# Kernel tuning notes

Hardware: AMD Instinct MI355X
Metric: run time of the kernel (lower is better)

Reference implementation:

```python
import jax, jax.numpy as jnp
import numpy as np

N_VAR, N_CON, N_SOC = 100_000, 100_000, 20_000
E_VC, E_SC = 2_000_000, 300_000
H = 64


def setup_inputs() -> dict:
    key = jax.random.key(0)
    ks = iter(jax.random.split(key, 64))

    def rn(shape, s=0.05):
        return jax.random.normal(next(ks), shape, jnp.float32) * s

    inp = {
        "var_x": rn((N_VAR, 7), 1.0),
        "con_x": rn((N_CON, 4), 1.0),
        "soc_x": rn((N_SOC, 6), 1.0),
        "W_var": rn((7, H)), "b_var": jnp.zeros((H,), jnp.float32),
        "W_con": rn((4, H)), "b_con": jnp.zeros((H,), jnp.float32),
        "W_soc": rn((6, H)), "b_soc": jnp.zeros((H,), jnp.float32),
    }
    for l in ("l1", "l2"):
        for d in ("f", "b"):
            inp[f"{l}{d}_Wp"] = rn((H, H))
            inp[f"{l}{d}_bp"] = jnp.zeros((H,), jnp.float32)
            inp[f"{l}{d}_Ws"] = rn((H, H))
            inp[f"{l}{d}_Wn"] = rn((H, H))
            inp[f"{l}{d}_b"] = jnp.zeros((H,), jnp.float32)
    inp["W_hid"] = rn((H, H)); inp["b_hid"] = jnp.zeros((H,), jnp.float32)
    inp["W_out"] = rn((H, 1)); inp["b_out"] = jnp.zeros((1,), jnp.float32)
    inp["vc_src"] = jax.random.randint(next(ks), (E_VC,), 0, N_VAR)
    inp["vc_dst"] = jax.random.randint(next(ks), (E_VC,), 0, N_CON)
    inp["sc_src"] = jax.random.randint(next(ks), (E_SC,), 0, N_SOC)
    inp["sc_dst"] = jax.random.randint(next(ks), (E_SC,), 0, N_CON)
    return inp


def _sage_pool(x_src, x_dst, src, dst, n_dst, Wp, bp, Ws, Wn, b):
    """DGL SAGEConv(aggregator_type='pool') on one bipartite relation.

    max-pool of relu(fc_pool(src feats)) over in-edges, then fc_self + fc_neigh + bias.
    """
    pooled = jax.nn.relu(x_src @ Wp + bp)                       # [N_src, H]
    agg = jax.ops.segment_max(pooled[src], dst, num_segments=n_dst)  # [N_dst, H]
    agg = jnp.where(jnp.isfinite(agg), agg, 0.0)                # zero in-degree -> 0 (DGL semantics)
    return x_dst @ Ws + agg @ Wn + b


def reference(var_x, con_x, soc_x,
              W_var, b_var, W_con, b_con, W_soc, b_soc,
              l1f_Wp, l1f_bp, l1f_Ws, l1f_Wn, l1f_b,
              l1b_Wp, l1b_bp, l1b_Ws, l1b_Wn, l1b_b,
              l2f_Wp, l2f_bp, l2f_Ws, l2f_Wn, l2f_b,
              l2b_Wp, l2b_bp, l2b_Ws, l2b_Wn, l2b_b,
              W_hid, b_hid, W_out, b_out,
              vc_src, vc_dst, sc_src, sc_dst):
    n_var, n_con, n_soc = var_x.shape[0], con_x.shape[0], soc_x.shape[0]

    # PreNormLayer with beta=0, sigma=1 (non-trainable, no pretrain update) is identity.
    h_var = jax.nn.relu(var_x @ W_var + b_var)
    h_con = jax.nn.relu(con_x @ W_con + b_con)
    h_soc = jax.nn.relu(soc_x @ W_soc + b_soc)

    # Each conv layer shares one SAGEConv for {v2c, s2c} and one for {c2v, c2s}.
    layers = [
        ((l1f_Wp, l1f_bp, l1f_Ws, l1f_Wn, l1f_b), (l1b_Wp, l1b_bp, l1b_Ws, l1b_Wn, l1b_b)),
        ((l2f_Wp, l2f_bp, l2f_Ws, l2f_Wn, l2f_b), (l2b_Wp, l2b_bp, l2b_Ws, l2b_Wn, l2b_b)),
    ]

    # n_passes = 1
    # forward half-pass: update constraint nodes; HeteroGraphConv sums v2c and s2c outputs.
    for fwd, _ in layers:
        c = (_sage_pool(h_var, h_con, vc_src, vc_dst, n_con, *fwd)
             + _sage_pool(h_soc, h_con, sc_src, sc_dst, n_con, *fwd))
        h_con = jax.nn.relu(c)
    # backward half-pass: update var and soc nodes from constraints (c2v, c2s = reversed edges).
    for _, bwd in layers:
        v = _sage_pool(h_con, h_var, vc_dst, vc_src, n_var, *bwd)
        s = _sage_pool(h_con, h_soc, sc_dst, sc_src, n_soc, *bwd)
        h_var = jax.nn.relu(v)
        h_soc = jax.nn.relu(s)

    # Output MLP: [Linear, ReLU]*2 in the source duplicates ONE shared Linear module.
    z = h_var
    for _ in range(2):
        z = jax.nn.relu(z @ W_hid + b_hid)
    return z @ W_out + b_out  # [n_var, 1] per-variable logits (readout_op=None)
```

## Files before the change

kernel.cpp:

```cpp
#include <hip/hip_runtime.h>

#define NV 100000
#define NC 100000
#define NSOC 20000
#define NVS (NV + NSOC)
#define EVC 2000000
#define ESC 300000
#define H 64

constexpr int BSH = 7;
constexpr int NBMAX = 1024;
constexpr int EPB = 8192;

template<int K1, int NSEC, bool RELU, int TR>
__global__ __launch_bounds__(256) void gemm_lds(
    const float* X1, const float* __restrict__ W1,
    const float* __restrict__ X2, const float* __restrict__ W2,
    const float* __restrict__ bias, float* out,
    int N, float s1)
{
  __shared__ __align__(16) float sx1[TR * K1];
  __shared__ __align__(16) float sx2[NSEC ? TR * H : 4];

  const int n0 = blockIdx.x * TR;

  if constexpr ((K1 & 3) == 0) {
    const float4* X4 = reinterpret_cast<const float4*>(X1);
    float4* S4 = reinterpret_cast<float4*>(sx1);
    const long base4 = (long)n0 * K1 / 4;
    const long lim4 = (long)N * K1 / 4;
    for (int i = threadIdx.x; i < TR * K1 / 4; i += 256)
      S4[i] = (base4 + i < lim4) ? X4[base4 + i] : make_float4(0.f, 0.f, 0.f, 0.f);
  } else {
    const long base = (long)n0 * K1;
    const long lim = (long)N * K1;
    for (int i = threadIdx.x; i < TR * K1; i += 256)
      sx1[i] = (base + i < lim) ? X1[base + i] : 0.f;
  }
  if constexpr (NSEC) {
    const float4* X4 = reinterpret_cast<const float4*>(X2);
    float4* S4 = reinterpret_cast<float4*>(sx2);
    const long base4 = (long)n0 * H / 4;
    const long lim4 = (long)N * H / 4;
    for (int i = threadIdx.x; i < TR * H / 4; i += 256)
      S4[i] = (base4 + i < lim4) ? X4[base4 + i] : make_float4(0.f, 0.f, 0.f, 0.f);
  }
  __syncthreads();

  const int lane = threadIdx.x & 63;
  const int wv = threadIdx.x >> 6;

  float w1[K1];
#pragma unroll
  for (int k = 0; k < K1; ++k) w1[k] = W1[k * H + lane];
  float w2[NSEC ? H : 1];
  if constexpr (NSEC) {
#pragma unroll
    for (int k = 0; k < H; ++k) w2[k] = W2[k * H + lane];
  }
  const float bj = bias[lane];

  constexpr int RPW = TR / 4;
  const int r0 = wv * RPW;

  if constexpr (K1 == H) {
    for (int i = 0; i < RPW; i += 2) {
      const int na = n0 + r0 + i;
      if (na >= N) break;
      const bool wb = (na + 1) < N;

      const float4* xa = reinterpret_cast<const float4*>(sx1 + (r0 + i) * H);
      const float4* xb = reinterpret_cast<const float4*>(sx1 + (r0 + i + 1) * H);
      float a0 = 0.f, a1 = 0.f, a2 = 0.f, a3 = 0.f;
      float b0 = 0.f, b1 = 0.f, b2 = 0.f, b3 = 0.f;
#pragma unroll
      for (int k4 = 0; k4 < H / 4; ++k4) {
        const float4 va = xa[k4];
        const float4 vb = xb[k4];
        a0 = fmaf(va.x, w1[4 * k4 + 0], a0);
        b0 = fmaf(vb.x, w1[4 * k4 + 0], b0);
        a1 = fmaf(va.y, w1[4 * k4 + 1], a1);
        b1 = fmaf(vb.y, w1[4 * k4 + 1], b1);
        a2 = fmaf(va.z, w1[4 * k4 + 2], a2);
        b2 = fmaf(vb.z, w1[4 * k4 + 2], b2);
        a3 = fmaf(va.w, w1[4 * k4 + 3], a3);
        b3 = fmaf(vb.w, w1[4 * k4 + 3], b3);
      }
      float accA = s1 * (((a0 + a1) + (a2 + a3)) + bj);
      float accB = s1 * (((b0 + b1) + (b2 + b3)) + bj);

      if constexpr (NSEC) {
        const float4* ya = reinterpret_cast<const float4*>(sx2 + (r0 + i) * H);
        const float4* yb = reinterpret_cast<const float4*>(sx2 + (r0 + i + 1) * H);
        a0 = 0.f; a1 = 0.f; a2 = 0.f; a3 = 0.f;
        b0 = 0.f; b1 = 0.f; b2 = 0.f; b3 = 0.f;
#pragma unroll
        for (int k4 = 0; k4 < H / 4; ++k4) {
          const float4 va = ya[k4];
          const float4 vb = yb[k4];
          a0 = fmaf(va.x, w2[4 * k4 + 0], a0);
          b0 = fmaf(vb.x, w2[4 * k4 + 0], b0);
          a1 = fmaf(va.y, w2[4 * k4 + 1], a1);
          b1 = fmaf(vb.y, w2[4 * k4 + 1], b1);
          a2 = fmaf(va.z, w2[4 * k4 + 2], a2);
          b2 = fmaf(vb.z, w2[4 * k4 + 2], b2);
          a3 = fmaf(va.w, w2[4 * k4 + 3], a3);
          b3 = fmaf(vb.w, w2[4 * k4 + 3], b3);
        }
        accA += (a0 + a1) + (a2 + a3);
        accB += (b0 + b1) + (b2 + b3);
      }

      if constexpr (RELU) { accA = fmaxf(accA, 0.f); accB = fmaxf(accB, 0.f); }
      out[(size_t)na * H + lane] = accA;
      if (wb) out[(size_t)(na + 1) * H + lane] = accB;
    }
  } else {
    for (int i = 0; i < RPW; i += 2) {
      const int na = n0 + r0 + i;
      if (na >= N) break;
      const bool wb = (na + 1) < N;
      const float* xa = sx1 + (r0 + i) * K1;
      const float* xb = sx1 + (r0 + i + 1) * K1;
      float accA = 0.f, accB = 0.f;
#pragma unroll
      for (int k = 0; k < K1; ++k) {
        accA = fmaf(xa[k], w1[k], accA);
        accB = fmaf(xb[k], w1[k], accB);
      }
      accA = s1 * (accA + bj);
      accB = s1 * (accB + bj);
      if constexpr (RELU) { accA = fmaxf(accA, 0.f); accB = fmaxf(accB, 0.f); }
      out[(size_t)na * H + lane] = accA;
      if (wb) out[(size_t)(na + 1) * H + lane] = accB;
    }
  }
}

template<int TR>
__global__ __launch_bounds__(256) void dualgemm_k(
    const float* __restrict__ X, const float* __restrict__ Wa,
    const float* __restrict__ ba, const float* __restrict__ Wb,
    const float* __restrict__ bb, float* __restrict__ out, int N)
{
  __shared__ __align__(16) float sx[TR * H];
  const int n0 = blockIdx.x * TR;
  {
    const float4* X4 = reinterpret_cast<const float4*>(X);
    float4* S4 = reinterpret_cast<float4*>(sx);
    const long base4 = (long)n0 * (H / 4);
    const long lim4 = (long)N * (H / 4);
    for (int i = threadIdx.x; i < TR * H / 4; i += 256)
      S4[i] = (base4 + i < lim4) ? X4[base4 + i] : make_float4(0.f, 0.f, 0.f, 0.f);
  }
  __syncthreads();

  const int lane = threadIdx.x & 63;
  const int wv = threadIdx.x >> 6;
  float wA[H], wB[H];
#pragma unroll
  for (int k = 0; k < H; ++k) { wA[k] = Wa[k * H + lane]; wB[k] = Wb[k * H + lane]; }
  const float bja = ba[lane];
  const float bjb = bb[lane];

  constexpr int RPW = TR / 4;
  const int r0 = wv * RPW;
  for (int i = 0; i < RPW; i += 2) {
    const int na = n0 + r0 + i;
    if (na >= N) break;
    const bool hasB = (na + 1) < N;

    const float4* xa = reinterpret_cast<const float4*>(sx + (r0 + i) * H);
    const float4* xb = reinterpret_cast<const float4*>(sx + (r0 + i + 1) * H);
    float pa0 = 0.f, pa1 = 0.f, pa2 = 0.f, pa3 = 0.f;
    float pb0 = 0.f, pb1 = 0.f, pb2 = 0.f, pb3 = 0.f;
    float qa0 = 0.f, qa1 = 0.f, qa2 = 0.f, qa3 = 0.f;
    float qb0 = 0.f, qb1 = 0.f, qb2 = 0.f, qb3 = 0.f;
#pragma unroll
    for (int k4 = 0; k4 < H / 4; ++k4) {
      const float4 va = xa[k4];
      const float4 vb = xb[k4];
      pa0 = fmaf(va.x, wA[4 * k4 + 0], pa0);
      pb0 = fmaf(vb.x, wA[4 * k4 + 0], pb0);
      qa0 = fmaf(va.x, wB[4 * k4 + 0], qa0);
      qb0 = fmaf(vb.x, wB[4 * k4 + 0], qb0);
      pa1 = fmaf(va.y, wA[4 * k4 + 1], pa1);
      pb1 = fmaf(vb.y, wA[4 * k4 + 1], pb1);
      qa1 = fmaf(va.y, wB[4 * k4 + 1], qa1);
      qb1 = fmaf(vb.y, wB[4 * k4 + 1], qb1);
      pa2 = fmaf(va.z, wA[4 * k4 + 2], pa2);
      pb2 = fmaf(vb.z, wA[4 * k4 + 2], pb2);
      qa2 = fmaf(va.z, wB[4 * k4 + 2], qa2);
      qb2 = fmaf(vb.z, wB[4 * k4 + 2], qb2);
      pa3 = fmaf(va.w, wA[4 * k4 + 3], pa3);
      pb3 = fmaf(vb.w, wA[4 * k4 + 3], pb3);
      qa3 = fmaf(va.w, wB[4 * k4 + 3], qa3);
      qb3 = fmaf(vb.w, wB[4 * k4 + 3], qb3);
    }
    const float accAa = fmaxf((pa0 + pa1) + (pa2 + pa3) + bja, 0.f);
    const float accAb = fmaxf((qa0 + qa1) + (qa2 + qa3) + bjb, 0.f);
    out[(size_t)na * 128 + lane] = accAa;
    out[(size_t)na * 128 + 64 + lane] = accAb;
    if (hasB) {
      const float accBa = fmaxf((pb0 + pb1) + (pb2 + pb3) + bja, 0.f);
      const float accBb = fmaxf((qb0 + qb1) + (qb2 + qb3) + bjb, 0.f);
      out[(size_t)(na + 1) * 128 + lane] = accBa;
      out[(size_t)(na + 1) * 128 + 64 + lane] = accBb;
    }
  }
}

template<int TR>
__global__ __launch_bounds__(256) void mlp_k(
    const float* __restrict__ X, const float* __restrict__ W,
    const float* __restrict__ bh, const float* __restrict__ Wout,
    const float* __restrict__ bo, float* __restrict__ out, int N)
{
  __shared__ __align__(16) float sx[TR * H];
  __shared__ __align__(16) float sz[4][H];

  const int n0 = blockIdx.x * TR;
  {
    const float4* X4 = reinterpret_cast<const float4*>(X);
    float4* S4 = reinterpret_cast<float4*>(sx);
    const long base4 = (long)n0 * H / 4;
    const long lim4 = (long)N * H / 4;
    for (int i = threadIdx.x; i < TR * H / 4; i += 256)
      S4[i] = (base4 + i < lim4) ? X4[base4 + i] : make_float4(0.f, 0.f, 0.f, 0.f);
  }
  __syncthreads();

  const int lane = threadIdx.x & 63;
  const int wv = threadIdx.x >> 6;
  float w[H];
#pragma unroll
  for (int k = 0; k < H; ++k) w[k] = W[k * H + lane];
  const float bhl = bh[lane];
  const float wo = Wout[lane];
  const float bol = bo[0];

  constexpr int RPW = TR / 4;
  const int r0 = wv * RPW;
  for (int i = 0; i < RPW; ++i) {
    const int n = n0 + r0 + i;
    if (n >= N) break;
    const float4* x4 = reinterpret_cast<const float4*>(sx + (r0 + i) * H);
    float a0 = 0.f, a1 = 0.f, a2 = 0.f, a3 = 0.f;
#pragma unroll
    for (int k4 = 0; k4 < H / 4; ++k4) {
      const float4 v = x4[k4];
      a0 = fmaf(v.x, w[4 * k4 + 0], a0);
      a1 = fmaf(v.y, w[4 * k4 + 1], a1);
      a2 = fmaf(v.z, w[4 * k4 + 2], a2);
      a3 = fmaf(v.w, w[4 * k4 + 3], a3);
    }
    const float z1 = fmaxf((a0 + a1) + (a2 + a3) + bhl, 0.f);
    sz[wv][lane] = z1;
    const float4* z4 = reinterpret_cast<const float4*>(sz[wv]);
    a0 = 0.f; a1 = 0.f; a2 = 0.f; a3 = 0.f;
#pragma unroll
    for (int k4 = 0; k4 < H / 4; ++k4) {
      const float4 v = z4[k4];
      a0 = fmaf(v.x, w[4 * k4 + 0], a0);
      a1 = fmaf(v.y, w[4 * k4 + 1], a1);
      a2 = fmaf(v.z, w[4 * k4 + 2], a2);
      a3 = fmaf(v.w, w[4 * k4 + 3], a3);
    }
    const float z2 = fmaxf((a0 + a1) + (a2 + a3) + bhl, 0.f);
    float v = z2 * wo;
#pragma unroll
    for (int off = 32; off; off >>= 1) v += __shfl_down(v, off);
    if (lane == 0) out[n] = v + bol;
  }
}

__global__ __launch_bounds__(256) void bhist_k(const int* __restrict__ key,
                                               int* __restrict__ bcnt, int E, int nb) {
  __shared__ int h[NBMAX];
  for (int i = threadIdx.x; i < nb; i += 256) h[i] = 0;
  __syncthreads();
  const int base = blockIdx.x * EPB;
  for (int i = threadIdx.x; i < EPB; i += 256) {
    const int e = base + i;
    if (e < E) atomicAdd(&h[key[e] >> BSH], 1);
  }
  __syncthreads();
  for (int i = threadIdx.x; i < nb; i += 256)
    if (h[i]) atomicAdd(&bcnt[i], h[i]);
}

__global__ __launch_bounds__(1024) void bscan_k(const int* __restrict__ bcnt,
                                                int* __restrict__ bcur,
                                                int* __restrict__ sbase, int nb) {
  __shared__ int s[1024];
  const int t = threadIdx.x;
  const int v = (t < nb) ? bcnt[t] : 0;
  s[t] = v;
  __syncthreads();
  for (int off = 1; off < 1024; off <<= 1) {
    int x = (t >= off) ? s[t - off] : 0;
    __syncthreads();
    s[t] += x;
    __syncthreads();
  }
  if (t < nb) {
    const int ex = s[t] - v;
    bcur[t] = ex;
    sbase[t] = ex;
    if (t == nb - 1) sbase[nb] = s[t];
  }
}

__global__ __launch_bounds__(256) void bscatter_k(
    const int* __restrict__ key, const int* __restrict__ payload,
    int* __restrict__ bcur, int2* __restrict__ sorted, int E, int nb) {
  __shared__ int h[NBMAX];
  __shared__ int gb[NBMAX];
  __shared__ unsigned short lr[EPB];
  for (int i = threadIdx.x; i < nb; i += 256) h[i] = 0;
  __syncthreads();
  const int base = blockIdx.x * EPB;
  for (int i = threadIdx.x; i < EPB; i += 256) {
    const int e = base + i;
    if (e < E) lr[i] = (unsigned short)atomicAdd(&h[key[e] >> BSH], 1);
  }
  __syncthreads();
  for (int i = threadIdx.x; i < nb; i += 256)
    if (h[i]) gb[i] = atomicAdd(&bcur[i], h[i]);
  __syncthreads();
  for (int i = threadIdx.x; i < EPB; i += 256) {
    const int e = base + i;
    if (e < E) {
      const int k = key[e];
      sorted[gb[k >> BSH] + lr[i]] = make_int2(k, payload[e]);
    }
  }
}

__global__ __launch_bounds__(256) void bfinish_k(
    const int2* __restrict__ sorted, const int* __restrict__ sbase,
    int* __restrict__ rp, int* __restrict__ ei, int Nn) {
  __shared__ int cnt[128];
  __shared__ int scn[128];
  const int b = blockIdx.x;
  const int node0 = b << BSH;
  const int e0 = sbase[b], e1 = sbase[b + 1];
  const int t = threadIdx.x;
  if (t < 128) cnt[t] = 0;
  __syncthreads();
  for (int e = e0 + t; e < e1; e += 256)
    atomicAdd(&cnt[sorted[e].x - node0], 1);
  __syncthreads();
  if (t < 128) scn[t] = cnt[t];
  __syncthreads();
#pragma unroll
  for (int off = 1; off < 128; off <<= 1) {
    int v = (t < 128 && t >= off) ? scn[t - off] : 0;
    __syncthreads();
    if (t < 128) scn[t] += v;
    __syncthreads();
  }
  const int nInB = (Nn - node0 < 128) ? (Nn - node0) : 128;
  int myexcl = 0;
  if (t < 128) myexcl = scn[t] - cnt[t];
  if (t < nInB) rp[node0 + t] = e0 + myexcl;
  if (b == (int)gridDim.x - 1 && t == 0) rp[Nn] = e1;
  __syncthreads();
  if (t < 128) cnt[t] = myexcl;
  __syncthreads();
  for (int e = e0 + t; e < e1; e += 256) {
    const int2 kp = sorted[e];
    const int p = atomicAdd(&cnt[kp.x - node0], 1);
    ei[e0 + p] = kp.y;
  }
}

__device__ __forceinline__ float4 fmax4(float4 a, float4 b) {
  return make_float4(fmaxf(a.x, b.x), fmaxf(a.y, b.y),
                     fmaxf(a.z, b.z), fmaxf(a.w, b.w));
}

__device__ __forceinline__ float4 gmax2_csr(const float4* __restrict__ t4,
                                            const int* __restrict__ rp,
                                            const int* __restrict__ ei,
                                            int n, int g, int sub) {
  const int p0 = rp[n], p1 = rp[n + 1];
  const float4 z = make_float4(0.f, 0.f, 0.f, 0.f);
  float4 m0 = z, m1 = z, m2 = z, m3 = z, m4 = z, m5 = z, m6 = z, m7 = z;
  if (p1 > p0) {
    const int last = p1 - 1;
    for (int p = p0; p < p1; p += 16) {
      int e0 = p + 0 + g;  e0 = e0 <= last ? e0 : last;
      int e1 = p + 2 + g;  e1 = e1 <= last ? e1 : last;
      int e2 = p + 4 + g;  e2 = e2 <= last ? e2 : last;
      int e3 = p + 6 + g;  e3 = e3 <= last ? e3 : last;
      int e4 = p + 8 + g;  e4 = e4 <= last ? e4 : last;
      int e5 = p + 10 + g; e5 = e5 <= last ? e5 : last;
      int e6 = p + 12 + g; e6 = e6 <= last ? e6 : last;
      int e7 = p + 14 + g; e7 = e7 <= last ? e7 : last;
      const int s0 = ei[e0], s1 = ei[e1], s2 = ei[e2], s3 = ei[e3];
      const int s4 = ei[e4], s5 = ei[e5], s6 = ei[e6], s7 = ei[e7];
      m0 = fmax4(m0, t4[(size_t)s0 * 32 + sub]);
      m1 = fmax4(m1, t4[(size_t)s1 * 32 + sub]);
      m2 = fmax4(m2, t4[(size_t)s2 * 32 + sub]);
      m3 = fmax4(m3, t4[(size_t)s3 * 32 + sub]);
      m4 = fmax4(m4, t4[(size_t)s4 * 32 + sub]);
      m5 = fmax4(m5, t4[(size_t)s5 * 32 + sub]);
      m6 = fmax4(m6, t4[(size_t)s6 * 32 + sub]);
      m7 = fmax4(m7, t4[(size_t)s7 * 32 + sub]);
    }
  }
  float4 m = fmax4(fmax4(fmax4(m0, m1), fmax4(m2, m3)),
                   fmax4(fmax4(m4, m5), fmax4(m6, m7)));
  m.x = fmaxf(m.x, __shfl_xor(m.x, 32));
  m.y = fmaxf(m.y, __shfl_xor(m.y, 32));
  m.z = fmaxf(m.z, __shfl_xor(m.z, 32));
  m.w = fmaxf(m.w, __shfl_xor(m.w, 32));
  return m;
}

__global__ __launch_bounds__(256) void gather2f_k(
    const float4* __restrict__ t4,
    const int* __restrict__ rpCv, const int* __restrict__ eiCv,
    const int* __restrict__ rpCs, const int* __restrict__ eiCs,
    float4* __restrict__ agg1, float4* __restrict__ agg2, int N)
{
  const int lane = threadIdx.x & 63;
  const int g = lane >> 5, sub = lane & 31;
  const int n = __builtin_amdgcn_readfirstlane(blockIdx.x * 4 + (threadIdx.x >> 6));
  if (n >= N) return;
  const float4 a = gmax2_csr(t4, rpCv, eiCv, n, g, sub);
  const float4 b = gmax2_csr(t4 + (size_t)NV * 32, rpCs, eiCs, n, g, sub);
  const float4 r = make_float4(a.x + b.x, a.y + b.y, a.z + b.z, a.w + b.w);
  if (g == 0) {
    if (sub < 16) agg1[(size_t)n * 16 + sub] = r;
    else          agg2[(size_t)n * 16 + (sub - 16)] = r;
  }
}

__global__ __launch_bounds__(256) void gathervs2_k(
    const float4* __restrict__ t4,
    const int* __restrict__ rpV, const int* __restrict__ eiV,
    const int* __restrict__ rpS, const int* __restrict__ eiS,
    float4* __restrict__ agg1, float4* __restrict__ agg2)
{
  const int lane = threadIdx.x & 63;
  const int g = lane >> 5, sub = lane & 31;
  const int n = __builtin_amdgcn_readfirstlane(blockIdx.x * 4 + (threadIdx.x >> 6));
  if (n >= NVS) return;
  float4 m;
  if (n < NV) m = gmax2_csr(t4, rpV, eiV, n, g, sub);
  else        m = gmax2_csr(t4, rpS, eiS, n - NV, g, sub);
  if (g == 0) {
    if (sub < 16) agg1[(size_t)n * 16 + sub] = m;
    else          agg2[(size_t)n * 16 + (sub - 16)] = m;
  }
}

extern "C" void kernel_launch(void* const* d_in, const int* in_sizes, int n_in,
                              void* d_out, int out_size, void* d_ws, size_t ws_size,
                              hipStream_t stream) {
  const float* var_x = (const float*)d_in[0];
  const float* con_x = (const float*)d_in[1];
  const float* soc_x = (const float*)d_in[2];
  const float* W_var = (const float*)d_in[3];
  const float* b_var = (const float*)d_in[4];
  const float* W_con = (const float*)d_in[5];
  const float* b_con = (const float*)d_in[6];
  const float* W_soc = (const float*)d_in[7];
  const float* b_soc = (const float*)d_in[8];
  const float* L[4][5];
  for (int l = 0; l < 4; ++l)
    for (int p = 0; p < 5; ++p)
      L[l][p] = (const float*)d_in[9 + l * 5 + p];
  const float* W_hid = (const float*)d_in[29];
  const float* b_hid = (const float*)d_in[30];
  const float* W_out = (const float*)d_in[31];
  const float* b_out = (const float*)d_in[32];
  const int* vc_src = (const int*)d_in[33];
  const int* vc_dst = (const int*)d_in[34];
  const int* sc_src = (const int*)d_in[35];
  const int* sc_dst = (const int*)d_in[36];

  char* ws = (char*)d_ws;
  const size_t F_VS = (size_t)NVS * H * 4;
  const size_t F_C  = (size_t)NC * H * 4;
  float* hvs   = (float*)(ws);
  float* h_con = (float*)(ws + F_VS);
  float* bufA  = (float*)(ws + F_VS + F_C);
  float* bufB  = (float*)(ws + 3 * F_VS + F_C);
  int2*  sorted = (int2*)bufB;
  char* csr = ws + 3 * F_VS + 3 * F_C;
  int* rpCv = (int*)(csr);
  int* eiCv = rpCv + (NC + 1);
  int* rpCs = eiCv + EVC;
  int* eiCs = rpCs + (NC + 1);
  int* rpV  = eiCs + ESC;
  int* eiV  = rpV + (NV + 1);
  int* rpS  = eiV + EVC;
  int* eiS  = rpS + (NSOC + 1);
  int* aux  = eiS + ESC;
  int* bcnt[4];
  for (int i = 0; i < 4; ++i) bcnt[i] = aux + i * 1024;
  int* bcur  = aux + 4 * 1024;
  int* sbase = aux + 5 * 1024;

  constexpr int TR = 64;
  auto grid_l = [](int n) { return dim3((unsigned)((n + TR - 1) / TR)); };
  auto grid_w = [](int n) { return dim3((unsigned)((n + 3) / 4)); };
  auto grid_b = [](int e) { return dim3((unsigned)((e + EPB - 1) / EPB)); };
  const dim3 B(256);

  float* h_var = hvs;
  float* h_soc = hvs + (size_t)NV * H;

  hipMemsetAsync(aux, 0, 4 * 1024 * sizeof(int), stream);

  auto build_csr = [&](const int* key, const int* payload, int E, int Nn,
                       int* rp, int* ei, int bi) {
    const int nb = (Nn + (1 << BSH) - 1) >> BSH;
    bhist_k<<<grid_b(E), B, 0, stream>>>(key, bcnt[bi], E, nb);
    bscan_k<<<dim3(1), dim3(1024), 0, stream>>>(bcnt[bi], bcur, sbase, nb);
    bscatter_k<<<grid_b(E), B, 0, stream>>>(key, payload, bcur, sorted, E, nb);
    bfinish_k<<<dim3((unsigned)nb), B, 0, stream>>>(sorted, sbase, rp, ei, Nn);
  };

  build_csr(vc_dst, vc_src, EVC, NC, rpCv, eiCv, 0);
  build_csr(sc_dst, sc_src, ESC, NC, rpCs, eiCs, 1);
  build_csr(vc_src, vc_dst, EVC, NV, rpV, eiV, 2);
  build_csr(sc_src, sc_dst, ESC, NSOC, rpS, eiS, 3);

  gemm_lds<7, 0, true, TR><<<grid_l(NV), B, 0, stream>>>(var_x, W_var, nullptr, nullptr, b_var, h_var, NV, 1.f);
  gemm_lds<4, 0, true, TR><<<grid_l(NC), B, 0, stream>>>(con_x, W_con, nullptr, nullptr, b_con, h_con, NC, 1.f);
  gemm_lds<6, 0, true, TR><<<grid_l(NSOC), B, 0, stream>>>(soc_x, W_soc, nullptr, nullptr, b_soc, h_soc, NSOC, 1.f);

  float* agg1f = bufB;
  float* agg2f = bufB + (size_t)NC * H;
  dualgemm_k<TR><<<grid_l(NVS), B, 0, stream>>>(hvs, L[0][0], L[0][1], L[2][0], L[2][1], bufA, NVS);
  gather2f_k<<<grid_w(NC), B, 0, stream>>>((const float4*)bufA, rpCv, eiCv, rpCs, eiCs,
                                           (float4*)agg1f, (float4*)agg2f, NC);
  gemm_lds<64, 1, true, TR><<<grid_l(NC), B, 0, stream>>>(h_con, L[0][2], agg1f, L[0][3], L[0][4], h_con, NC, 2.f);
  gemm_lds<64, 1, true, TR><<<grid_l(NC), B, 0, stream>>>(h_con, L[2][2], agg2f, L[2][3], L[2][4], h_con, NC, 2.f);

  float* agg1b = bufA;
  float* agg2b = bufA + (size_t)NVS * H;
  dualgemm_k<TR><<<grid_l(NC), B, 0, stream>>>(h_con, L[1][0], L[1][1], L[3][0], L[3][1], bufB, NC);
  gathervs2_k<<<grid_w(NVS), B, 0, stream>>>((const float4*)bufB, rpV, eiV, rpS, eiS,
                                             (float4*)agg1b, (float4*)agg2b);
  gemm_lds<64, 1, true, TR><<<grid_l(NVS), B, 0, stream>>>(hvs, L[1][2], agg1b, L[1][3], L[1][4], hvs, NVS, 1.f);
  gemm_lds<64, 1, true, TR><<<grid_l(NVS), B, 0, stream>>>(hvs, L[3][2], agg2b, L[3][3], L[3][4], hvs, NVS, 1.f);

  mlp_k<TR><<<grid_l(NV), B, 0, stream>>>(hvs, W_hid, b_hid, W_out, b_out, (float*)d_out, NV);
}
```

Before: 832.6 us.

## Merge VC CSR builds into one pass and skip dead soc backward update

```diff
diff --git a/kernel.cpp b/kernel.cpp
--- a/kernel.cpp
+++ b/kernel.cpp
@@ -11,30 +11,31 @@
 constexpr int BSH = 7;
 constexpr int NBMAX = 1024;
 constexpr int EPB = 8192;
-
-template<int K1, int NSEC, bool RELU, int TR>
+constexpr int TR = 64;
+
+template<int K1, int NSEC, bool RELU, int TRr>
 __global__ __launch_bounds__(256) void gemm_lds(
     const float* X1, const float* __restrict__ W1,
     const float* __restrict__ X2, const float* __restrict__ W2,
     const float* __restrict__ bias, float* out,
     int N, float s1)
 {
-  __shared__ __align__(16) float sx1[TR * K1];
-  __shared__ __align__(16) float sx2[NSEC ? TR * H : 4];
-
-  const int n0 = blockIdx.x * TR;
+  __shared__ __align__(16) float sx1[TRr * K1];
+  __shared__ __align__(16) float sx2[NSEC ? TRr * H : 4];
+
+  const int n0 = blockIdx.x * TRr;
 
   if constexpr ((K1 & 3) == 0) {
     const float4* X4 = reinterpret_cast<const float4*>(X1);
     float4* S4 = reinterpret_cast<float4*>(sx1);
     const long base4 = (long)n0 * K1 / 4;
     const long lim4 = (long)N * K1 / 4;
-    for (int i = threadIdx.x; i < TR * K1 / 4; i += 256)
+    for (int i = threadIdx.x; i < TRr * K1 / 4; i += 256)
       S4[i] = (base4 + i < lim4) ? X4[base4 + i] : make_float4(0.f, 0.f, 0.f, 0.f);
   } else {
     const long base = (long)n0 * K1;
     const long lim = (long)N * K1;
-    for (int i = threadIdx.x; i < TR * K1; i += 256)
+    for (int i = threadIdx.x; i < TRr * K1; i += 256)
       sx1[i] = (base + i < lim) ? X1[base + i] : 0.f;
   }
   if constexpr (NSEC) {
@@ -42,7 +43,7 @@
     float4* S4 = reinterpret_cast<float4*>(sx2);
     const long base4 = (long)n0 * H / 4;
     const long lim4 = (long)N * H / 4;
-    for (int i = threadIdx.x; i < TR * H / 4; i += 256)
+    for (int i = threadIdx.x; i < TRr * H / 4; i += 256)
       S4[i] = (base4 + i < lim4) ? X4[base4 + i] : make_float4(0.f, 0.f, 0.f, 0.f);
   }
   __syncthreads();
@@ -60,7 +61,7 @@
   }
   const float bj = bias[lane];
 
-  constexpr int RPW = TR / 4;
+  constexpr int RPW = TRr / 4;
   const int r0 = wv * RPW;
 
   if constexpr (K1 == H) {
@@ -137,20 +138,20 @@
   }
 }
 
-template<int TR>
+template<int TRr>
 __global__ __launch_bounds__(256) void dualgemm_k(
     const float* __restrict__ X, const float* __restrict__ Wa,
     const float* __restrict__ ba, const float* __restrict__ Wb,
     const float* __restrict__ bb, float* __restrict__ out, int N)
 {
-  __shared__ __align__(16) float sx[TR * H];
-  const int n0 = blockIdx.x * TR;
+  __shared__ __align__(16) float sx[TRr * H];
+  const int n0 = blockIdx.x * TRr;
   {
     const float4* X4 = reinterpret_cast<const float4*>(X);
     float4* S4 = reinterpret_cast<float4*>(sx);
     const long base4 = (long)n0 * (H / 4);
     const long lim4 = (long)N * (H / 4);
-    for (int i = threadIdx.x; i < TR * H / 4; i += 256)
+    for (int i = threadIdx.x; i < TRr * H / 4; i += 256)
       S4[i] = (base4 + i < lim4) ? X4[base4 + i] : make_float4(0.f, 0.f, 0.f, 0.f);
   }
   __syncthreads();
@@ -163,7 +164,7 @@
   const float bja = ba[lane];
   const float bjb = bb[lane];
 
-  constexpr int RPW = TR / 4;
+  constexpr int RPW = TRr / 4;
   const int r0 = wv * RPW;
   for (int i = 0; i < RPW; i += 2) {
     const int na = n0 + r0 + i;
@@ -197,35 +198,31 @@
       qa3 = fmaf(va.w, wB[4 * k4 + 3], qa3);
       qb3 = fmaf(vb.w, wB[4 * k4 + 3], qb3);
     }
-    const float accAa = fmaxf((pa0 + pa1) + (pa2 + pa3) + bja, 0.f);
-    const float accAb = fmaxf((qa0 + qa1) + (qa2 + qa3) + bjb, 0.f);
-    out[(size_t)na * 128 + lane] = accAa;
-    out[(size_t)na * 128 + 64 + lane] = accAb;
+    out[(size_t)na * 128 + lane] = fmaxf((pa0 + pa1) + (pa2 + pa3) + bja, 0.f);
+    out[(size_t)na * 128 + 64 + lane] = fmaxf((qa0 + qa1) + (qa2 + qa3) + bjb, 0.f);
     if (hasB) {
-      const float accBa = fmaxf((pb0 + pb1) + (pb2 + pb3) + bja, 0.f);
-      const float accBb = fmaxf((qb0 + qb1) + (qb2 + qb3) + bjb, 0.f);
-      out[(size_t)(na + 1) * 128 + lane] = accBa;
-      out[(size_t)(na + 1) * 128 + 64 + lane] = accBb;
-    }
-  }
-}
-
-template<int TR>
+      out[(size_t)(na + 1) * 128 + lane] = fmaxf((pb0 + pb1) + (pb2 + pb3) + bja, 0.f);
+      out[(size_t)(na + 1) * 128 + 64 + lane] = fmaxf((qb0 + qb1) + (qb2 + qb3) + bjb, 0.f);
+    }
+  }
+}
+
+template<int TRr>
 __global__ __launch_bounds__(256) void mlp_k(
     const float* __restrict__ X, const float* __restrict__ W,
     const float* __restrict__ bh, const float* __restrict__ Wout,
     const float* __restrict__ bo, float* __restrict__ out, int N)
 {
-  __shared__ __align__(16) float sx[TR * H];
+  __shared__ __align__(16) float sx[TRr * H];
   __shared__ __align__(16) float sz[4][H];
 
-  const int n0 = blockIdx.x * TR;
+  const int n0 = blockIdx.x * TRr;
   {
     const float4* X4 = reinterpret_cast<const float4*>(X);
     float4* S4 = reinterpret_cast<float4*>(sx);
     const long base4 = (long)n0 * H / 4;
     const long lim4 = (long)N * H / 4;
-    for (int i = threadIdx.x; i < TR * H / 4; i += 256)
+    for (int i = threadIdx.x; i < TRr * H / 4; i += 256)
       S4[i] = (base4 + i < lim4) ? X4[base4 + i] : make_float4(0.f, 0.f, 0.f, 0.f);
   }
   __syncthreads();
@@ -239,7 +236,7 @@
   const float wo = Wout[lane];
   const float bol = bo[0];
 
-  constexpr int RPW = TR / 4;
+  constexpr int RPW = TRr / 4;
   const int r0 = wv * RPW;
   for (int i = 0; i < RPW; ++i) {
     const int n = n0 + r0 + i;
@@ -274,10 +271,30 @@
   }
 }
 
+__global__ __launch_bounds__(256) void bhist2_k(
+    const int* __restrict__ kD, const int* __restrict__ kS,
+    int* __restrict__ bcntD, int* __restrict__ bcntS, int E, int nbD, int nbS)
+{
+  __shared__ int hD[NBMAX], hS[NBMAX];
+  for (int i = threadIdx.x; i < NBMAX; i += 256) { hD[i] = 0; hS[i] = 0; }
+  __syncthreads();
+  const int base = blockIdx.x * EPB;
+  for (int i = threadIdx.x; i < EPB; i += 256) {
+    const int e = base + i;
+    if (e < E) {
+      atomicAdd(&hD[kD[e] >> BSH], 1);
+      atomicAdd(&hS[kS[e] >> BSH], 1);
+    }
+  }
+  __syncthreads();
+  for (int i = threadIdx.x; i < nbD; i += 256) if (hD[i]) atomicAdd(&bcntD[i], hD[i]);
+  for (int i = threadIdx.x; i < nbS; i += 256) if (hS[i]) atomicAdd(&bcntS[i], hS[i]);
+}
+
 __global__ __launch_bounds__(256) void bhist_k(const int* __restrict__ key,
                                                int* __restrict__ bcnt, int E, int nb) {
   __shared__ int h[NBMAX];
-  for (int i = threadIdx.x; i < nb; i += 256) h[i] = 0;
+  for (int i = threadIdx.x; i < NBMAX; i += 256) h[i] = 0;
   __syncthreads();
   const int base = blockIdx.x * EPB;
   for (int i = threadIdx.x; i < EPB; i += 256) {
@@ -289,12 +306,11 @@
     if (h[i]) atomicAdd(&bcnt[i], h[i]);
 }
 
-__global__ __launch_bounds__(1024) void bscan_k(const int* __restrict__ bcnt,
-                                                int* __restrict__ bcur,
-                                                int* __restrict__ sbase, int nb) {
-  __shared__ int s[1024];
+__device__ __forceinline__ void scan_dev(const int* __restrict__ cnt,
+                                         int* __restrict__ cur,
+                                         int* __restrict__ sbase, int nb, int* s) {
   const int t = threadIdx.x;
-  const int v = (t < nb) ? bcnt[t] : 0;
+  const int v = (t < nb) ? cnt[t] : 0;
   s[t] = v;
   __syncthreads();
   for (int off = 1; off < 1024; off <<= 1) {
@@ -305,9 +321,55 @@
   }
   if (t < nb) {
     const int ex = s[t] - v;
-    bcur[t] = ex;
+    cur[t] = ex;
     sbase[t] = ex;
     if (t == nb - 1) sbase[nb] = s[t];
+  }
+  __syncthreads();
+}
+
+__global__ __launch_bounds__(1024) void bscan2_k(
+    const int* __restrict__ cD, int* __restrict__ curD, int* __restrict__ sbD, int nbD,
+    const int* __restrict__ cS, int* __restrict__ curS, int* __restrict__ sbS, int nbS) {
+  __shared__ int s[1024];
+  scan_dev(cD, curD, sbD, nbD, s);
+  scan_dev(cS, curS, sbS, nbS, s);
+}
+
+__global__ __launch_bounds__(1024) void bscan1_k(
+    const int* __restrict__ c, int* __restrict__ cur, int* __restrict__ sb, int nb) {
+  __shared__ int s[1024];
+  scan_dev(c, cur, sb, nb, s);
+}
+
+__global__ __launch_bounds__(256) void bscatter2_k(
+    const int* __restrict__ kD, const int* __restrict__ kS,
+    int* __restrict__ bcurD, int* __restrict__ bcurS,
+    int2* __restrict__ sortedD, int2* __restrict__ sortedS, int E, int nbD, int nbS)
+{
+  __shared__ int hD[NBMAX], gbD[NBMAX], hS[NBMAX], gbS[NBMAX];
+  __shared__ unsigned short lrD[EPB], lrS[EPB];
+  for (int i = threadIdx.x; i < NBMAX; i += 256) { hD[i] = 0; hS[i] = 0; }
+  __syncthreads();
+  const int base = blockIdx.x * EPB;
+  for (int i = threadIdx.x; i < EPB; i += 256) {
+    const int e = base + i;
+    if (e < E) {
+      lrD[i] = (unsigned short)atomicAdd(&hD[kD[e] >> BSH], 1);
+      lrS[i] = (unsigned short)atomicAdd(&hS[kS[e] >> BSH], 1);
+    }
+  }
+  __syncthreads();
+  for (int i = threadIdx.x; i < nbD; i += 256) if (hD[i]) gbD[i] = atomicAdd(&bcurD[i], hD[i]);
+  for (int i = threadIdx.x; i < nbS; i += 256) if (hS[i]) gbS[i] = atomicAdd(&bcurS[i], hS[i]);
+  __syncthreads();
+  for (int i = threadIdx.x; i < EPB; i += 256) {
+    const int e = base + i;
+    if (e < E) {
+      const int d = kD[e], s = kS[e];
+      sortedD[gbD[d >> BSH] + lrD[i]] = make_int2(d, s);
+      sortedS[gbS[s >> BSH] + lrS[i]] = make_int2(s, d);
+    }
   }
 }
 
@@ -317,7 +379,7 @@
   __shared__ int h[NBMAX];
   __shared__ int gb[NBMAX];
   __shared__ unsigned short lr[EPB];
-  for (int i = threadIdx.x; i < nb; i += 256) h[i] = 0;
+  for (int i = threadIdx.x; i < NBMAX; i += 256) h[i] = 0;
   __syncthreads();
   const int base = blockIdx.x * EPB;
   for (int i = threadIdx.x; i < EPB; i += 256) {
@@ -438,19 +500,16 @@
   }
 }
 
-__global__ __launch_bounds__(256) void gathervs2_k(
+__global__ __launch_bounds__(256) void gatherB_k(
     const float4* __restrict__ t4,
-    const int* __restrict__ rpV, const int* __restrict__ eiV,
-    const int* __restrict__ rpS, const int* __restrict__ eiS,
-    float4* __restrict__ agg1, float4* __restrict__ agg2)
+    const int* __restrict__ rp, const int* __restrict__ ei,
+    float4* __restrict__ agg1, float4* __restrict__ agg2, int N)
 {
   const int lane = threadIdx.x & 63;
   const int g = lane >> 5, sub = lane & 31;
   const int n = __builtin_amdgcn_readfirstlane(blockIdx.x * 4 + (threadIdx.x >> 6));
-  if (n >= NVS) return;
-  float4 m;
-  if (n < NV) m = gmax2_csr(t4, rpV, eiV, n, g, sub);
-  else        m = gmax2_csr(t4, rpS, eiS, n - NV, g, sub);
+  if (n >= N) return;
+  const float4 m = gmax2_csr(t4, rp, ei, n, g, sub);
   if (g == 0) {
     if (sub < 16) agg1[(size_t)n * 16 + sub] = m;
     else          agg2[(size_t)n * 16 + (sub - 16)] = m;
@@ -483,72 +542,76 @@
   const int* sc_dst = (const int*)d_in[36];
 
   char* ws = (char*)d_ws;
-  const size_t F_VS = (size_t)NVS * H * 4;
-  const size_t F_C  = (size_t)NC * H * 4;
-  float* hvs   = (float*)(ws);
-  float* h_con = (float*)(ws + F_VS);
-  float* bufA  = (float*)(ws + F_VS + F_C);
-  float* bufB  = (float*)(ws + 3 * F_VS + F_C);
-  int2*  sorted = (int2*)bufB;
-  char* csr = ws + 3 * F_VS + 3 * F_C;
-  int* rpCv = (int*)(csr);
+  const size_t SZ_HVS = (size_t)NVS * H * 4;
+  const size_t SZ_PF  = (size_t)NVS * 128 * 4;
+  const size_t SZ_AC  = (size_t)NC * H * 4;
+  const size_t SZ_PB  = (size_t)NC * 128 * 4;
+  float* h_vs    = (float*)ws;
+  float* pooledF = (float*)(ws + SZ_HVS);
+  float* agg1b   = pooledF;
+  float* agg2b   = pooledF + (size_t)NV * H;
+  float* agg1f   = (float*)(ws + SZ_HVS + SZ_PF);
+  float* agg2f   = agg1f + (size_t)NC * H;
+  float* h_con   = (float*)(ws + SZ_HVS + SZ_PF + 2 * SZ_AC);
+  float* pooledB = (float*)(ws + SZ_HVS + SZ_PF + 3 * SZ_AC);
+  int2*  sortedD = (int2*)pooledB;
+  int2*  sortedS = (int2*)((char*)pooledB + (size_t)EVC * 8);
+  int* csr = (int*)(ws + SZ_HVS + SZ_PF + 3 * SZ_AC + SZ_PB);
+  int* rpCv = csr;
   int* eiCv = rpCv + (NC + 1);
   int* rpCs = eiCv + EVC;
   int* eiCs = rpCs + (NC + 1);
   int* rpV  = eiCs + ESC;
   int* eiV  = rpV + (NV + 1);
-  int* rpS  = eiV + EVC;
-  int* eiS  = rpS + (NSOC + 1);
-  int* aux  = eiS + ESC;
-  int* bcnt[4];
-  for (int i = 0; i < 4; ++i) bcnt[i] = aux + i * 1024;
-  int* bcur  = aux + 4 * 1024;
-  int* sbase = aux + 5 * 1024;
-
-  constexpr int TR = 64;
+  int* aux  = eiV + EVC;
+  int* bcntD = aux;
+  int* bcntS = aux + 1024;
+  int* bcntC = aux + 2048;
+  int* bcurD = aux + 3072;
+  int* bcurS = aux + 4096;
+  int* bcurC = aux + 5120;
+  int* sbD   = aux + 6144;
+  int* sbS   = sbD + 1056;
+  int* sbC   = sbS + 1056;
+
+  const int nbC = (NC + 127) >> BSH;
+  const int nbV = (NV + 127) >> BSH;
   auto grid_l = [](int n) { return dim3((unsigned)((n + TR - 1) / TR)); };
   auto grid_w = [](int n) { return dim3((unsigned)((n + 3) / 4)); };
   auto grid_b = [](int e) { return dim3((unsigned)((e + EPB - 1) / EPB)); };
   const dim3 B(256);
 
-  float* h_var = hvs;
-  float* h_soc = hvs + (size_t)NV * H;
-
-  hipMemsetAsync(aux, 0, 4 * 1024 * sizeof(int), stream);
-
-  auto build_csr = [&](const int* key, const int* payload, int E, int Nn,
-                       int* rp, int* ei, int bi) {
-    const int nb = (Nn + (1 << BSH) - 1) >> BSH;
-    bhist_k<<<grid_b(E), B, 0, stream>>>(key, bcnt[bi], E, nb);
-    bscan_k<<<dim3(1), dim3(1024), 0, stream>>>(bcnt[bi], bcur, sbase, nb);
-    bscatter_k<<<grid_b(E), B, 0, stream>>>(key, payload, bcur, sorted, E, nb);
-    bfinish_k<<<dim3((unsigned)nb), B, 0, stream>>>(sorted, sbase, rp, ei, Nn);
-  };
-
-  build_csr(vc_dst, vc_src, EVC, NC, rpCv, eiCv, 0);
-  build_csr(sc_dst, sc_src, ESC, NC, rpCs, eiCs, 1);
-  build_csr(vc_src, vc_dst, EVC, NV, rpV, eiV, 2);
-  build_csr(sc_src, sc_dst, ESC, NSOC, rpS, eiS, 3);
+  float* h_var = h_vs;
+  float* h_soc = h_vs + (size_t)NV * H;
+
+  hipMemsetAsync(aux, 0, 3072 * sizeof(int), stream);
+
+  bhist2_k<<<grid_b(EVC), B, 0, stream>>>(vc_dst, vc_src, bcntD, bcntS, EVC, nbC, nbV);
+  bscan2_k<<<dim3(1), dim3(1024), 0, stream>>>(bcntD, bcurD, sbD, nbC, bcntS, bcurS, sbS, nbV);
+  bscatter2_k<<<grid_b(EVC), B, 0, stream>>>(vc_dst, vc_src, bcurD, bcurS, sortedD, sortedS, EVC, nbC, nbV);
+  bfinish_k<<<dim3((unsigned)nbC), B, 0, stream>>>(sortedD, sbD, rpCv, eiCv, NC);
+  bfinish_k<<<dim3((unsigned)nbV), B, 0, stream>>>(sortedS, sbS, rpV, eiV, NV);
+  bhist_k<<<grid_b(ESC), B, 0, stream>>>(sc_dst, bcntC, ESC, nbC);
+  bscan1_k<<<dim3(1), dim3(1024), 0, stream>>>(bcntC, bcurC, sbC, nbC);
+  bscatter_k<<<grid_b(ESC), B, 0, stream>>>(sc_dst, sc_src, bcurC, sortedD, ESC, nbC);
+  bfinish_k<<<dim3((unsigned)nbC), B, 0, stream>>>(sortedD, sbC, rpCs, eiCs, NC);
 
   gemm_lds<7, 0, true, TR><<<grid_l(NV), B, 0, stream>>>(var_x, W_var, nullptr, nullptr, b_var, h_var, NV, 1.f);
   gemm_lds<4, 0, true, TR><<<grid_l(NC), B, 0, stream>>>(con_x, W_con, nullptr, nullptr, b_con, h_con, NC, 1.f);
   gemm_lds<6, 0, true, TR><<<grid_l(NSOC), B, 0, stream>>>(soc_x, W_soc, nullptr, nullptr, b_soc, h_soc, NSOC, 1.f);
 
-  float* agg1f = bufB;
-  float* agg2f = bufB + (size_t)NC * H;
-  dualgemm_k<TR><<<grid_l(NVS), B, 0, stream>>>(hvs, L[0][0], L[0][1], L[2][0], L[2][1], bufA, NVS);
-  gather2f_k<<<grid_w(NC), B, 0, stream>>>((const float4*)bufA, rpCv, eiCv, rpCs, eiCs,
-                                           (float4*)agg1f, (float4*)agg2f, NC);
+  dualgemm_k<TR><<<grid_l(NVS), B, 0, stream>>>(h_vs, L[0][0], L[0][1], L[2][0], L[2][1], pooledF, NVS);
+  gather2f_k<<<grid_w(NC), B, 0, stream>>>(
+      (const float4*)pooledF, rpCv, eiCv, rpCs, eiCs,
+      (float4*)agg1f, (float4*)agg2f, NC);
   gemm_lds<64, 1, true, TR><<<grid_l(NC), B, 0, stream>>>(h_con, L[0][2], agg1f, L[0][3], L[0][4], h_con, NC, 2.f);
   gemm_lds<64, 1, true, TR><<<grid_l(NC), B, 0, stream>>>(h_con, L[2][2], agg2f, L[2][3], L[2][4], h_con, NC, 2.f);
 
-  float* agg1b = bufA;
-  float* agg2b = bufA + (size_t)NVS * H;
-  dualgemm_k<TR><<<grid_l(NC), B, 0, stream>>>(h_con, L[1][0], L[1][1], L[3][0], L[3][1], bufB, NC);
-  gathervs2_k<<<grid_w(NVS), B, 0, stream>>>((const float4*)bufB, rpV, eiV, rpS, eiS,
-                                             (float4*)agg1b, (float4*)agg2b);
-  gemm_lds<64, 1, true, TR><<<grid_l(NVS), B, 0, stream>>>(hvs, L[1][2], agg1b, L[1][3], L[1][4], hvs, NVS, 1.f);
-  gemm_lds<64, 1, true, TR><<<grid_l(NVS), B, 0, stream>>>(hvs, L[3][2], agg2b, L[3][3], L[3][4], hvs, NVS, 1.f);
-
-  mlp_k<TR><<<grid_l(NV), B, 0, stream>>>(hvs, W_hid, b_hid, W_out, b_out, (float*)d_out, NV);
-}
+  dualgemm_k<TR><<<grid_l(NC), B, 0, stream>>>(h_con, L[1][0], L[1][1], L[3][0], L[3][1], pooledB, NC);
+  gatherB_k<<<grid_w(NV), B, 0, stream>>>(
+      (const float4*)pooledB, rpV, eiV, (float4*)agg1b, (float4*)agg2b, NV);
+  gemm_lds<64, 1, true, TR><<<grid_l(NV), B, 0, stream>>>(h_var, L[1][2], agg1b, L[1][3], L[1][4], h_var, NV, 1.f);
+  gemm_lds<64, 1, true, TR><<<grid_l(NV), B, 0, stream>>>(h_var, L[3][2], agg2b, L[3][3], L[3][4], h_var, NV, 1.f);
+
+  mlp_k<TR><<<grid_l(NV), B, 0, stream>>>(h_var, W_hid, b_hid, W_out, b_out, (float*)d_out, NV);
+}
```

Measured after the change: 754.1 us, median of 2. 1.1x faster.
